# Kernel optimization log

Hardware: AMD Instinct MI355X
Metric: run time of the kernel (lower is better)

Reference implementation:

```python
import jax, jax.numpy as jnp
import numpy as np

E, H, I = 8, 1024, 1024  # num_local_experts, hidden_size, intermediate_size
T = 4096                 # tokens (batch*seq)
ALPHA, LIMIT = 1.702, 7.0


def setup_inputs() -> dict:
    key = jax.random.key(0)
    ks = jax.random.split(key, 6)
    return {
        "hidden_states": jax.random.normal(ks[0], (T, H), dtype=jnp.float32),
        "routing_weights": jax.random.uniform(ks[1], (T, E), dtype=jnp.float32),
        "gate_up_proj": jax.random.normal(ks[2], (E, H, 2 * I), dtype=jnp.float32) * 0.02,
        "gate_up_proj_bias": jax.random.normal(ks[3], (E, 2 * I), dtype=jnp.float32) * 0.02,
        "down_proj": jax.random.normal(ks[4], (E, H, I), dtype=jnp.float32) * 0.02,
        "down_proj_bias": jax.random.normal(ks[5], (E, I), dtype=jnp.float32) * 0.02,
    }


def reference(hidden_states, routing_weights, gate_up_proj, gate_up_proj_bias,
              down_proj, down_proj_bias):
    # Dense all-experts path (GPT-OSS Experts forward).
    # gate_up: [E, T, 2I]
    gate_up = jnp.einsum('th,ehf->etf', hidden_states, gate_up_proj) + gate_up_proj_bias[:, None, :]
    gate = gate_up[..., ::2]   # interleaved split
    up = gate_up[..., 1::2]
    gate = jnp.minimum(gate, LIMIT)
    up = jnp.clip(up, -LIMIT, LIMIT)
    glu = gate * jax.nn.sigmoid(gate * ALPHA)
    act = (up + 1.0) * glu     # [E, T, I]
    # down_proj declared [E, H, I] -> contract over I
    out_e = jnp.einsum('eti,ehi->eth', act, down_proj) + down_proj_bias[:, None, :]  # [E, T, H]
    out = jnp.einsum('eth,te->th', out_e, routing_weights)  # [T, H]
    return out
```

## Files before the change

### kernel.cpp

```cpp
#include <hip/hip_runtime.h>
#include <hip/hip_bf16.h>
#include <stdint.h>

#define T_DIM 4096
#define H_DIM 1024
#define I_DIM 1024
#define E_DIM 8
#define F_DIM 2048
#define K2_DIM 8192
#define ALPHA_C 1.702f
#define LIMIT_C 7.0f

typedef unsigned short u16;
typedef __bf16 bf8 __attribute__((ext_vector_type(8)));
typedef float f4 __attribute__((ext_vector_type(4)));

__device__ __forceinline__ u16 f2bf(float f) {
  union { float f; unsigned u; } x; x.f = f;
  unsigned r = (x.u + 0x7fffu + ((x.u >> 16) & 1u)) >> 16;
  return (u16)r;
}

__device__ __forceinline__ void gload16(const void* g, void* l) {
  __builtin_amdgcn_global_load_lds(
      (const __attribute__((address_space(1))) void*)g,
      (__attribute__((address_space(3))) void*)l,
      16, 0, 0);
}


__global__ void cast_bf16_kernel(const float* __restrict__ in, u16* __restrict__ out, int n4) {
  int idx = blockIdx.x * blockDim.x + threadIdx.x;
  int stride = gridDim.x * blockDim.x;
  for (int i = idx; i < n4; i += stride) {
    float4 v = reinterpret_cast<const float4*>(in)[i];
    ushort4 o;
    o.x = f2bf(v.x); o.y = f2bf(v.y); o.z = f2bf(v.z); o.w = f2bf(v.w);
    reinterpret_cast<ushort4*>(out)[i] = o;
  }
}

__global__ void cast_transpose_gup(const float* __restrict__ in, u16* __restrict__ out) {
  __shared__ float tile[32][33];
  int e = blockIdx.z, h0 = blockIdx.y * 32, f0 = blockIdx.x * 32;
  int tx = threadIdx.x & 31, ty = threadIdx.x >> 5;
  const float* src = in + (size_t)e * H_DIM * F_DIM;
  u16* dst = out + (size_t)e * F_DIM * H_DIM;
#pragma unroll
  for (int r = ty; r < 32; r += 8) tile[r][tx] = src[(size_t)(h0 + r) * F_DIM + f0 + tx];
  __syncthreads();
#pragma unroll
  for (int r = ty; r < 32; r += 8) dst[(size_t)(f0 + r) * H_DIM + h0 + tx] = f2bf(tile[tx][r]);
}


__global__ __launch_bounds__(256, 2) void gemm1_act(
    const u16* __restrict__ A,
    const u16* __restrict__ Bt,
    const float* __restrict__ rw,
    const float* __restrict__ gbias,
    u16* __restrict__ act2)
{
  const int e  = blockIdx.z;
  const int t0 = blockIdx.y * 128;
  const int n0 = blockIdx.x * 128;
  const int tid = threadIdx.x;
  const int w = tid >> 6, l = tid & 63;
  const int wr = w >> 1, wc = w & 1;

  __shared__ u16 As[128 * 32];
  __shared__ u16 Bs[128 * 32];
  __shared__ float rw_s[128];
  __shared__ float gb_s[128];

  if (tid < 128) {
    rw_s[tid] = rw[(size_t)(t0 + tid) * E_DIM + e];
    gb_s[tid] = gbias[(size_t)e * F_DIM + n0 + tid];
  }

  const u16* bBase = Bt + (size_t)e * F_DIM * H_DIM;

  f4 acc[4][4];
#pragma unroll
  for (int m = 0; m < 4; ++m)
#pragma unroll
    for (int n = 0; n < 4; ++n) acc[m][n] = f4{0.f, 0.f, 0.f, 0.f};

  const int row_st = l >> 2;
  const int col_st = (l & 3) * 8;

  for (int kt = 0; kt < H_DIM / 32; ++kt) {
    const int k0 = kt * 32;
    __syncthreads();
#pragma unroll
    for (int c = 0; c < 2; ++c) {
      int q = w * 2 + c;
      int row = q * 16 + row_st;
      gload16(A + (size_t)(t0 + row) * H_DIM + k0 + col_st, (char*)As + q * 1024);
      gload16(bBase + (size_t)(n0 + row) * H_DIM + k0 + col_st, (char*)Bs + q * 1024);
    }
    __syncthreads();

    bf8 af[4], bfr[4];
#pragma unroll
    for (int m = 0; m < 4; ++m) {
      int row = wr * 64 + m * 16 + (l & 15);
      af[m] = *(const bf8*)(As + row * 32 + (l >> 4) * 8);
    }
#pragma unroll
    for (int n = 0; n < 4; ++n) {
      int row = wc * 64 + n * 16 + (l & 15);
      bfr[n] = *(const bf8*)(Bs + row * 32 + (l >> 4) * 8);
    }
#pragma unroll
    for (int m = 0; m < 4; ++m)
#pragma unroll
      for (int n = 0; n < 4; ++n)
        acc[m][n] = __builtin_amdgcn_mfma_f32_16x16x32_bf16(af[m], bfr[n], acc[m][n], 0, 0, 0);
  }

#pragma unroll
  for (int m = 0; m < 4; ++m) {
#pragma unroll
    for (int n = 0; n < 4; ++n) {
#pragma unroll
      for (int r = 0; r < 4; ++r) {
        int row = wr * 64 + m * 16 + (l >> 4) * 4 + r;
        int col = wc * 64 + n * 16 + (l & 15);
        float v = acc[m][n][r] + gb_s[col];
        float o = __shfl_xor(v, 1, 64);
        float gate = (l & 1) ? o : v;
        float up   = (l & 1) ? v : o;
        gate = fminf(gate, LIMIT_C);
        up   = fminf(fmaxf(up, -LIMIT_C), LIMIT_C);
        float glu = gate / (1.f + __expf(-gate * ALPHA_C));
        float a = (up + 1.f) * glu * rw_s[row];
        if (!(l & 1)) {
          int i = (n0 + col) >> 1;
          act2[(size_t)(t0 + row) * K2_DIM + e * I_DIM + i] = f2bf(a);
        }
      }
    }
  }
}


__global__ __launch_bounds__(256, 2) void gemm2(
    const u16* __restrict__ A,
    const u16* __restrict__ Bt,
    const float* __restrict__ rw,
    const float* __restrict__ dbias,
    float* __restrict__ out)
{
  const int t0 = blockIdx.y * 128;
  const int n0 = blockIdx.x * 128;
  const int tid = threadIdx.x;
  const int w = tid >> 6, l = tid & 63;
  const int wr = w >> 1, wc = w & 1;

  __shared__ u16 As[128 * 32];
  __shared__ u16 Bs[128 * 32];
  __shared__ float rw_s[128 * 8];
  __shared__ float db_s[8 * 128];

  {
    reinterpret_cast<float4*>(rw_s)[tid] =
        reinterpret_cast<const float4*>(rw + (size_t)t0 * E_DIM)[tid];
    int idx0 = tid * 4;
    int ee = idx0 >> 7, c = idx0 & 127;
    reinterpret_cast<float4*>(db_s)[tid] =
        *reinterpret_cast<const float4*>(dbias + (size_t)ee * I_DIM + n0 + c);
  }

  f4 acc[4][4];
#pragma unroll
  for (int m = 0; m < 4; ++m)
#pragma unroll
    for (int n = 0; n < 4; ++n) acc[m][n] = f4{0.f, 0.f, 0.f, 0.f};

  const int row_st = l >> 2;
  const int col_st = (l & 3) * 8;

  for (int kt = 0; kt < K2_DIM / 32; ++kt) {
    const int k0 = kt * 32;
    const int eb = k0 >> 10;
    const int ki = k0 & 1023;
    __syncthreads();
#pragma unroll
    for (int c = 0; c < 2; ++c) {
      int q = w * 2 + c;
      int row = q * 16 + row_st;
      gload16(A + (size_t)(t0 + row) * K2_DIM + k0 + col_st, (char*)As + q * 1024);
      gload16(Bt + ((size_t)eb * H_DIM + n0 + row) * I_DIM + ki + col_st, (char*)Bs + q * 1024);
    }
    __syncthreads();

    bf8 af[4], bfr[4];
#pragma unroll
    for (int m = 0; m < 4; ++m) {
      int row = wr * 64 + m * 16 + (l & 15);
      af[m] = *(const bf8*)(As + row * 32 + (l >> 4) * 8);
    }
#pragma unroll
    for (int n = 0; n < 4; ++n) {
      int row = wc * 64 + n * 16 + (l & 15);
      bfr[n] = *(const bf8*)(Bs + row * 32 + (l >> 4) * 8);
    }
#pragma unroll
    for (int m = 0; m < 4; ++m)
#pragma unroll
      for (int n = 0; n < 4; ++n)
        acc[m][n] = __builtin_amdgcn_mfma_f32_16x16x32_bf16(af[m], bfr[n], acc[m][n], 0, 0, 0);
  }

#pragma unroll
  for (int m = 0; m < 4; ++m) {
#pragma unroll
    for (int n = 0; n < 4; ++n) {
#pragma unroll
      for (int r = 0; r < 4; ++r) {
        int row = wr * 64 + m * 16 + (l >> 4) * 4 + r;
        int col = wc * 64 + n * 16 + (l & 15);
        float rb = 0.f;
#pragma unroll
        for (int ee = 0; ee < 8; ++ee) rb += rw_s[row * 8 + ee] * db_s[ee * 128 + col];
        out[(size_t)(t0 + row) * H_DIM + n0 + col] = acc[m][n][r] + rb;
      }
    }
  }
}


extern "C" void kernel_launch(void* const* d_in, const int* in_sizes, int n_in,
                              void* d_out, int out_size, void* d_ws, size_t ws_size,
                              hipStream_t stream) {
  const float* hs  = (const float*)d_in[0];
  const float* rw  = (const float*)d_in[1];
  const float* gup = (const float*)d_in[2];
  const float* gub = (const float*)d_in[3];
  const float* dp  = (const float*)d_in[4];
  const float* db  = (const float*)d_in[5];
  float* out = (float*)d_out;
  char* ws = (char*)d_ws;

  u16* hs_bf = (u16*)(ws);
  u16* gupT  = (u16*)(ws + 8ll  * 1024 * 1024);
  u16* dp_bf = (u16*)(ws + 40ll * 1024 * 1024);
  u16* act2  = (u16*)(ws + 56ll * 1024 * 1024);

  cast_bf16_kernel<<<2048, 256, 0, stream>>>(hs, hs_bf, T_DIM * H_DIM / 4);
  cast_transpose_gup<<<dim3(F_DIM / 32, H_DIM / 32, E_DIM), 256, 0, stream>>>(gup, gupT);
  cast_bf16_kernel<<<2048, 256, 0, stream>>>(dp, dp_bf, E_DIM * H_DIM * I_DIM / 4);
  gemm1_act<<<dim3(F_DIM / 128, T_DIM / 128, E_DIM), 256, 0, stream>>>(hs_bf, gupT, rw, gub, act2);
  gemm2<<<dim3(H_DIM / 128, T_DIM / 128), 256, 0, stream>>>(act2, dp_bf, rw, db, out);
}
```

Baseline: 502.8 us.

## Split-K gemm2 with atomics, bias prefill kernel, and XOR-swizzled LDS layout

Splits the down-projection GEMM along K into four slices, raising its grid from 256 to 1024 blocks so the GPU is better filled. Partial results are combined with float atomicAdd into an output that a new kernel prefills with the routing-weighted down bias. Both GEMMs also apply an XOR swizzle to the LDS chunk layout to cut bank conflicts on fragment reads. The cost is atomic traffic, an extra launch and output pass, and nondeterministic summation order.

New measurement: 491.9 us. 2.2% less time.

```diff
diff --git a/kernel.cpp b/kernel.cpp
--- a/kernel.cpp
+++ b/kernel.cpp
@@ -51,6 +51,24 @@
   __syncthreads();
 #pragma unroll
   for (int r = ty; r < 32; r += 8) dst[(size_t)(f0 + r) * H_DIM + h0 + tx] = f2bf(tile[tx][r]);
+}
+
+__global__ void bias_init(const float* __restrict__ rw, const float* __restrict__ db,
+                          float* __restrict__ out) {
+  __shared__ float db_s[E_DIM][H_DIM];
+  for (int i = threadIdx.x; i < E_DIM * H_DIM; i += 256)
+    db_s[i >> 10][i & 1023] = db[i];
+  int t = blockIdx.x;
+  float r0[E_DIM];
+#pragma unroll
+  for (int e = 0; e < E_DIM; ++e) r0[e] = rw[(size_t)t * E_DIM + e];
+  __syncthreads();
+  for (int h = threadIdx.x; h < H_DIM; h += 256) {
+    float s = 0.f;
+#pragma unroll
+    for (int e = 0; e < E_DIM; ++e) s += r0[e] * db_s[e][h];
+    out[(size_t)t * H_DIM + h] = s;
+  }
 }
 
 
@@ -87,7 +105,7 @@
     for (int n = 0; n < 4; ++n) acc[m][n] = f4{0.f, 0.f, 0.f, 0.f};
 
   const int row_st = l >> 2;
-  const int col_st = (l & 3) * 8;
+  const int col_sw = (((l & 3) ^ ((l >> 3) & 3)) * 8);
 
   for (int kt = 0; kt < H_DIM / 32; ++kt) {
     const int k0 = kt * 32;
@@ -96,8 +114,8 @@
     for (int c = 0; c < 2; ++c) {
       int q = w * 2 + c;
       int row = q * 16 + row_st;
-      gload16(A + (size_t)(t0 + row) * H_DIM + k0 + col_st, (char*)As + q * 1024);
-      gload16(bBase + (size_t)(n0 + row) * H_DIM + k0 + col_st, (char*)Bs + q * 1024);
+      gload16(A + (size_t)(t0 + row) * H_DIM + k0 + col_sw, (char*)As + q * 1024);
+      gload16(bBase + (size_t)(n0 + row) * H_DIM + k0 + col_sw, (char*)Bs + q * 1024);
     }
     __syncthreads();
 
@@ -105,12 +123,14 @@
 #pragma unroll
     for (int m = 0; m < 4; ++m) {
       int row = wr * 64 + m * 16 + (l & 15);
-      af[m] = *(const bf8*)(As + row * 32 + (l >> 4) * 8);
+      int ch = (l >> 4) ^ ((row >> 1) & 3);
+      af[m] = *(const bf8*)(As + row * 32 + ch * 8);
     }
 #pragma unroll
     for (int n = 0; n < 4; ++n) {
       int row = wc * 64 + n * 16 + (l & 15);
-      bfr[n] = *(const bf8*)(Bs + row * 32 + (l >> 4) * 8);
+      int ch = (l >> 4) ^ ((row >> 1) & 3);
+      bfr[n] = *(const bf8*)(Bs + row * 32 + ch * 8);
     }
 #pragma unroll
     for (int m = 0; m < 4; ++m)
@@ -148,29 +168,17 @@
 __global__ __launch_bounds__(256, 2) void gemm2(
     const u16* __restrict__ A,
     const u16* __restrict__ Bt,
-    const float* __restrict__ rw,
-    const float* __restrict__ dbias,
     float* __restrict__ out)
 {
   const int t0 = blockIdx.y * 128;
   const int n0 = blockIdx.x * 128;
+  const int s  = blockIdx.z;
   const int tid = threadIdx.x;
   const int w = tid >> 6, l = tid & 63;
   const int wr = w >> 1, wc = w & 1;
 
   __shared__ u16 As[128 * 32];
   __shared__ u16 Bs[128 * 32];
-  __shared__ float rw_s[128 * 8];
-  __shared__ float db_s[8 * 128];
-
-  {
-    reinterpret_cast<float4*>(rw_s)[tid] =
-        reinterpret_cast<const float4*>(rw + (size_t)t0 * E_DIM)[tid];
-    int idx0 = tid * 4;
-    int ee = idx0 >> 7, c = idx0 & 127;
-    reinterpret_cast<float4*>(db_s)[tid] =
-        *reinterpret_cast<const float4*>(dbias + (size_t)ee * I_DIM + n0 + c);
-  }
 
   f4 acc[4][4];
 #pragma unroll
@@ -179,9 +187,11 @@
     for (int n = 0; n < 4; ++n) acc[m][n] = f4{0.f, 0.f, 0.f, 0.f};
 
   const int row_st = l >> 2;
-  const int col_st = (l & 3) * 8;
-
-  for (int kt = 0; kt < K2_DIM / 32; ++kt) {
+  const int col_sw = (((l & 3) ^ ((l >> 3) & 3)) * 8);
+
+  const int kt_beg = s * (K2_DIM / 32 / 4);
+  const int kt_end = kt_beg + (K2_DIM / 32 / 4);
+  for (int kt = kt_beg; kt < kt_end; ++kt) {
     const int k0 = kt * 32;
     const int eb = k0 >> 10;
     const int ki = k0 & 1023;
@@ -190,8 +200,8 @@
     for (int c = 0; c < 2; ++c) {
       int q = w * 2 + c;
       int row = q * 16 + row_st;
-      gload16(A + (size_t)(t0 + row) * K2_DIM + k0 + col_st, (char*)As + q * 1024);
-      gload16(Bt + ((size_t)eb * H_DIM + n0 + row) * I_DIM + ki + col_st, (char*)Bs + q * 1024);
+      gload16(A + (size_t)(t0 + row) * K2_DIM + k0 + col_sw, (char*)As + q * 1024);
+      gload16(Bt + ((size_t)eb * H_DIM + n0 + row) * I_DIM + ki + col_sw, (char*)Bs + q * 1024);
     }
     __syncthreads();
 
@@ -199,12 +209,14 @@
 #pragma unroll
     for (int m = 0; m < 4; ++m) {
       int row = wr * 64 + m * 16 + (l & 15);
-      af[m] = *(const bf8*)(As + row * 32 + (l >> 4) * 8);
+      int ch = (l >> 4) ^ ((row >> 1) & 3);
+      af[m] = *(const bf8*)(As + row * 32 + ch * 8);
     }
 #pragma unroll
     for (int n = 0; n < 4; ++n) {
       int row = wc * 64 + n * 16 + (l & 15);
-      bfr[n] = *(const bf8*)(Bs + row * 32 + (l >> 4) * 8);
+      int ch = (l >> 4) ^ ((row >> 1) & 3);
+      bfr[n] = *(const bf8*)(Bs + row * 32 + ch * 8);
     }
 #pragma unroll
     for (int m = 0; m < 4; ++m)
@@ -221,10 +233,7 @@
       for (int r = 0; r < 4; ++r) {
         int row = wr * 64 + m * 16 + (l >> 4) * 4 + r;
         int col = wc * 64 + n * 16 + (l & 15);
-        float rb = 0.f;
-#pragma unroll
-        for (int ee = 0; ee < 8; ++ee) rb += rw_s[row * 8 + ee] * db_s[ee * 128 + col];
-        out[(size_t)(t0 + row) * H_DIM + n0 + col] = acc[m][n][r] + rb;
+        atomicAdd(out + (size_t)(t0 + row) * H_DIM + n0 + col, acc[m][n][r]);
       }
     }
   }
@@ -251,6 +260,7 @@
   cast_bf16_kernel<<<2048, 256, 0, stream>>>(hs, hs_bf, T_DIM * H_DIM / 4);
   cast_transpose_gup<<<dim3(F_DIM / 32, H_DIM / 32, E_DIM), 256, 0, stream>>>(gup, gupT);
   cast_bf16_kernel<<<2048, 256, 0, stream>>>(dp, dp_bf, E_DIM * H_DIM * I_DIM / 4);
+  bias_init<<<T_DIM, 256, 0, stream>>>(rw, db, out);
   gemm1_act<<<dim3(F_DIM / 128, T_DIM / 128, E_DIM), 256, 0, stream>>>(hs_bf, gupT, rw, gub, act2);
-  gemm2<<<dim3(H_DIM / 128, T_DIM / 128), 256, 0, stream>>>(act2, dp_bf, rw, db, out);
-}
+  gemm2<<<dim3(H_DIM / 128, T_DIM / 128, 4), 256, 0, stream>>>(act2, dp_bf, out);
+}
```
